# Performance work log

Hardware: AMD Instinct MI355X
Metric: run time of the kernel (lower is better)

The kernel has to match this reference:

```python
import jax, jax.numpy as jnp
import numpy as np

NUM_HEADS = 16
EPS = 1e-5


def _layernorm(x, gamma, beta):
    # LayerNorm over last dim (head_dim), biased variance as in torch
    mu = jnp.mean(x, axis=-1, keepdims=True)
    var = jnp.mean(jnp.square(x - mu), axis=-1, keepdims=True)
    return (x - mu) * jax.lax.rsqrt(var + EPS) * gamma + beta


def setup_inputs() -> dict:
    key = jax.random.key(0)
    ks = jax.random.split(key, 10)
    B, T, C = 16, 2048, 1024
    Bk = 4
    Dh = C // NUM_HEADS
    w = 0.02
    return {
        "q": jax.random.normal(ks[0], (B, T, C), jnp.float32),
        "k": jax.random.normal(ks[1], (Bk, T, C), jnp.float32),
        "v": jax.random.normal(ks[2], (Bk, T, C), jnp.float32),
        "Wq": jax.random.normal(ks[3], (C, C), jnp.float32) * w,
        "Wk": jax.random.normal(ks[4], (C, C), jnp.float32) * w,
        "Wv": jax.random.normal(ks[5], (C, C), jnp.float32) * w,
        "Wo": jax.random.normal(ks[6], (C, C), jnp.float32) * w,
        "bo": jnp.zeros((C,), jnp.float32),
        "gamma": jnp.ones((Dh,), jnp.float32),
        "beta": jnp.zeros((Dh,), jnp.float32),
    }


def reference(q, k, v, Wq, Wk, Wv, Wo, bo, gamma, beta):
    B, N, C = q.shape
    H = NUM_HEADS
    Dh = C // H
    scale = 8.0 / Dh  # use_mup=True

    reps = B // k.shape[0]
    k = jnp.tile(k, (reps, 1, 1))[:, :N]
    v = jnp.tile(v, (reps, 1, 1))[:, :N]

    # torch Linear: x @ W.T  (no qkv bias)
    qp = jnp.einsum("bnc,dc->bnd", q, Wq).reshape(B, N, H, Dh)
    kp = jnp.einsum("bnc,dc->bnd", k, Wk).reshape(B, N, H, Dh)
    vp = jnp.einsum("bnc,dc->bnd", v, Wv).reshape(B, N, H, Dh)

    qp = _layernorm(qp, gamma, beta) * scale
    kp = _layernorm(kp, gamma, beta)

    # Faithful to source: NO head permute before matmul -> per-token (H,H) attention
    attn = jnp.einsum("bnhd,bngd->bnhg", qp, kp)  # [B,N,H,H]
    attn = jax.nn.softmax(attn, axis=-1)
    x = jnp.einsum("bnhg,bngd->bnhd", attn, vp)  # [B,N,H,Dh]
    # torch: transpose(1,2).reshape(B,N,C)
    x = x.transpose(0, 2, 1, 3).reshape(B, N, C)
    return jnp.einsum("bnc,dc->bnd", x, Wo) + bo
```

## Files before the change

kernel.cpp:

```cpp
#include <hip/hip_runtime.h>
#include <stdint.h>

typedef short bf16x8 __attribute__((ext_vector_type(8)));
typedef float f32x4 __attribute__((ext_vector_type(4)));

#define DEVINL static __device__ __forceinline__
#define SB() __builtin_amdgcn_sched_barrier(0)

DEVINL unsigned short f2bf(float f) {
    union { float f; uint32_t u; } v; v.f = f;
    return (unsigned short)((v.u + 0x7FFFu + ((v.u >> 16) & 1u)) >> 16);
}
DEVINL float bf2f(unsigned short b) {
    union { uint32_t u; float f; } v; v.u = ((uint32_t)b) << 16;
    return v.f;
}

DEVINL void load_lds16(const void* g, void* l) {
    __builtin_amdgcn_global_load_lds(
        (const __attribute__((address_space(1))) void*)g,
        (__attribute__((address_space(3))) void*)l, 16, 0, 0);
}

__global__ __launch_bounds__(256) void k_cvtall(
    const float* __restrict__ q, const float* __restrict__ k, const float* __restrict__ v,
    const float* __restrict__ w0, const float* __restrict__ w1,
    const float* __restrict__ w2, const float* __restrict__ w3,
    unsigned short* __restrict__ dq, unsigned short* __restrict__ dk,
    unsigned short* __restrict__ dv,
    unsigned short* __restrict__ dw0, unsigned short* __restrict__ dw1,
    unsigned short* __restrict__ dw2, unsigned short* __restrict__ dw3)
{
    const float* src; unsigned short* dst; int n4, blk, nblk;
    const int b = blockIdx.x;
    if (b < 2048)      { src = q; dst = dq; n4 = 8388608; blk = b;        nblk = 2048; }
    else if (b < 2560) { src = k; dst = dk; n4 = 2097152; blk = b - 2048; nblk = 512; }
    else if (b < 3072) { src = v; dst = dv; n4 = 2097152; blk = b - 2560; nblk = 512; }
    else {
        const int wsel = (b - 3072) >> 6;
        const float* ws_[4] = {w0, w1, w2, w3};
        unsigned short* wd_[4] = {dw0, dw1, dw2, dw3};
        src = ws_[wsel]; dst = wd_[wsel]; n4 = 262144; blk = (b - 3072) & 63; nblk = 64;
    }
    for (int i = blk * 256 + threadIdx.x; i < n4; i += nblk * 256) {
        float4 f = reinterpret_cast<const float4*>(src)[i];
        ushort4 o;
        o.x = f2bf(f.x); o.y = f2bf(f.y); o.z = f2bf(f.z); o.w = f2bf(f.w);
        reinterpret_cast<ushort4*>(dst)[i] = o;
    }
}

#define MFMA_QUAD(mi, nj, av, bv)                                              \
    __builtin_amdgcn_s_setprio(1);                                             \
    _Pragma("unroll")                                                          \
    for (int i = 0; i < 4; ++i)                                                \
        _Pragma("unroll")                                                      \
        for (int j = 0; j < 2; ++j)                                            \
            _Pragma("unroll")                                                  \
            for (int ks = 0; ks < 2; ++ks)                                     \
                acc[(mi) * 4 + i][(nj) * 2 + j] =                              \
                    __builtin_amdgcn_mfma_f32_16x16x32_bf16(                   \
                        av[i][ks], bv[j][ks], acc[(mi)*4+i][(nj)*2+j], 0, 0, 0); \
    __builtin_amdgcn_s_setprio(0);

template<int EPI>
DEVINL void epi_write(f32x4 (&acc)[8][4], void* Cout,
                      const float* bias, const float* gamma, const float* beta,
                      int m0, int n0, int wr, int wc, int lane, int wg)
{
    constexpr int N = 1024;
    const int rr = lane & 15;
    const int rg = lane >> 4;
    if constexpr (EPI == 0) {
        #pragma unroll
        for (int jj = 0; jj < 4; ++jj) {
            const int col = n0 + wc * 64 + jj * 16 + rr;
            const float bv = bias[col];
            #pragma unroll
            for (int i = 0; i < 8; ++i) {
                const int row0 = m0 + wr * 128 + i * 16 + rg * 4;
                #pragma unroll
                for (int r = 0; r < 4; ++r)
                    reinterpret_cast<float*>(Cout)[(size_t)(row0 + r) * N + col] =
                        acc[i][jj][r] + bv;
            }
        }
    } else if constexpr (EPI == 1 || EPI == 3) {
        const float scale = (EPI == 1) ? 0.125f : 1.0f;
        float gm[4], bt[4];
        #pragma unroll
        for (int jj = 0; jj < 4; ++jj) { gm[jj] = gamma[jj * 16 + rr]; bt[jj] = beta[jj * 16 + rr]; }
        #pragma unroll
        for (int i = 0; i < 8; ++i)
            #pragma unroll
            for (int r = 0; r < 4; ++r) {
                float s = 0.f, sq = 0.f;
                #pragma unroll
                for (int jj = 0; jj < 4; ++jj) {
                    const float v = acc[i][jj][r];
                    s += v; sq += v * v;
                }
                s  += __shfl_xor(s, 1);  s  += __shfl_xor(s, 2);
                s  += __shfl_xor(s, 4);  s  += __shfl_xor(s, 8);
                sq += __shfl_xor(sq, 1); sq += __shfl_xor(sq, 2);
                sq += __shfl_xor(sq, 4); sq += __shfl_xor(sq, 8);
                const float mu = s * 0.015625f;
                const float var = sq * 0.015625f - mu * mu;
                const float inv = rsqrtf(var + 1e-5f);
                const int row = m0 + wr * 128 + i * 16 + rg * 4 + r;
                #pragma unroll
                for (int jj = 0; jj < 4; ++jj) {
                    const int col = n0 + wc * 64 + jj * 16 + rr;
                    const float val = ((acc[i][jj][r] - mu) * inv * gm[jj] + bt[jj]) * scale;
                    reinterpret_cast<unsigned short*>(Cout)[(size_t)row * N + col] = f2bf(val);
                }
            }
    } else {
        const int g = (wg & 3) * 4 + wc;
        const int kqv = g >> 3;
        const int ev = g & 7;
        #pragma unroll
        for (int i = 0; i < 8; ++i)
            #pragma unroll
            for (int r = 0; r < 4; ++r) {
                const int t = m0 + wr * 128 + i * 16 + rg * 4 + r;
                #pragma unroll
                for (int jj = 0; jj < 4; ++jj)
                    reinterpret_cast<unsigned short*>(Cout)[
                        (size_t)t * 1024 + jj * 256 + kqv * 128 + rr * 8 + ev] =
                        f2bf(acc[i][jj][r]);
            }
    }
}

#define LOFF(buf, ab, ks, row) (((((buf) * 2 + (ab)) * 2 + (ks)) * 256 + (row)) * 32)

template<int EPI>
DEVINL void gemm256_body(
    const unsigned short* __restrict__ A,
    const unsigned short* __restrict__ B,
    void* __restrict__ Cout,
    const float* __restrict__ bias,
    const float* __restrict__ gamma,
    const float* __restrict__ beta,
    unsigned short* lds, int bid, int nwg, int tid)
{
    constexpr int K = 1024;
    constexpr int NT = 16;

    const int wg  = (bid & 7) * (nwg >> 3) + (bid >> 3);
    const int m0 = (wg >> 2) * 256;
    const int n0 = (wg & 3) * 256;

    const int w = tid >> 6;
    const int lane = tid & 63;
    const int wr = w >> 2;
    const int wc = w & 3;

    const int srow = lane >> 2;
    const int sseg = lane & 3;
    const int sslot = sseg ^ ((srow >> 1) & 3);

    f32x4 acc[8][4] = {};

    auto stage_unit = [&](int buf, int kt, int unit) {
        const int k0 = kt * 64;
        const int ab = unit & 1;
        const int sel = unit >> 1;
        #pragma unroll
        for (int j = 0; j < 2; ++j) {
            const int c  = (w << 1) | j;
            const int ks = c >> 3;
            const int c3 = c & 7;
            const int rg = ab ? (sel * 2 + (c3 & 1) + ((c3 >> 1) << 2))
                              : (sel * 4 + (c3 & 3) + ((c3 >> 2) << 3));
            const int row = rg * 16 + srow;
            const unsigned short* src =
                (ab ? B + (size_t)(n0 + row) * K : A + (size_t)(m0 + row) * K)
                + k0 + ks * 32 + sslot * 8;
            load_lds16(src, lds + LOFF(buf, ab, ks, rg * 16));
        }
    };

    const int rr = lane & 15;
    const int rdslot = ((lane >> 4) ^ ((rr >> 1) & 3)) * 8;

    auto rd_a = [&](bf16x8 (&dst)[4][2], int cur, int mh) {
        #pragma unroll
        for (int i = 0; i < 4; ++i)
            #pragma unroll
            for (int ks = 0; ks < 2; ++ks)
                dst[i][ks] = *reinterpret_cast<const bf16x8*>(
                    lds + LOFF(cur, 0, ks, wr * 128 + mh * 64 + i * 16 + rr) + rdslot);
    };
    auto rd_b = [&](bf16x8 (&dst)[2][2], int cur, int nh) {
        #pragma unroll
        for (int j = 0; j < 2; ++j)
            #pragma unroll
            for (int ks = 0; ks < 2; ++ks)
                dst[j][ks] = *reinterpret_cast<const bf16x8*>(
                    lds + LOFF(cur, 1, ks, wc * 64 + nh * 32 + j * 16 + rr) + rdslot);
    };

    stage_unit(0, 0, 0);
    stage_unit(0, 0, 1);
    stage_unit(0, 0, 3);
    stage_unit(0, 0, 2);
    asm volatile("s_waitcnt vmcnt(4)" ::: "memory");
    __builtin_amdgcn_s_barrier();
    SB();

    bf16x8 a[4][2], b0[2][2], b1[2][2];
    int cur = 0;
    for (int kt = 0; kt < NT - 1; ++kt) {
        const int nxt = cur ^ 1;

        rd_a(a, cur, 0);
        rd_b(b0, cur, 0);
        SB();
        stage_unit(nxt, kt + 1, 0);
        asm volatile("s_waitcnt vmcnt(4)" ::: "memory");
        __builtin_amdgcn_s_barrier();
        SB();
        asm volatile("s_waitcnt lgkmcnt(0)" ::: "memory");
        SB();
        MFMA_QUAD(0, 0, a, b0)

        rd_b(b1, cur, 1);
        SB();
        stage_unit(nxt, kt + 1, 1);
        asm volatile("s_waitcnt vmcnt(4)" ::: "memory");
        __builtin_amdgcn_s_barrier();
        SB();
        asm volatile("s_waitcnt lgkmcnt(0)" ::: "memory");
        SB();
        MFMA_QUAD(0, 1, a, b1)

        rd_a(a, cur, 1);
        SB();
        stage_unit(nxt, kt + 1, 3);
        __builtin_amdgcn_s_barrier();
        SB();
        asm volatile("s_waitcnt lgkmcnt(0)" ::: "memory");
        SB();
        MFMA_QUAD(1, 0, a, b0)

        stage_unit(nxt, kt + 1, 2);
        asm volatile("s_waitcnt vmcnt(4)" ::: "memory");
        __builtin_amdgcn_s_barrier();
        SB();
        MFMA_QUAD(1, 1, a, b1)
        cur = nxt;
    }

    {
        rd_a(a, cur, 0);
        rd_b(b0, cur, 0);
        SB();
        asm volatile("s_waitcnt vmcnt(2)" ::: "memory");
        __builtin_amdgcn_s_barrier();
        SB();
        asm volatile("s_waitcnt lgkmcnt(0)" ::: "memory");
        SB();
        MFMA_QUAD(0, 0, a, b0)

        rd_b(b1, cur, 1);
        SB();
        asm volatile("s_waitcnt vmcnt(0)" ::: "memory");
        __builtin_amdgcn_s_barrier();
        SB();
        asm volatile("s_waitcnt lgkmcnt(0)" ::: "memory");
        SB();
        MFMA_QUAD(0, 1, a, b1)

        rd_a(a, cur, 1);
        SB();
        asm volatile("s_waitcnt lgkmcnt(0)" ::: "memory");
        SB();
        MFMA_QUAD(1, 0, a, b0)
        MFMA_QUAD(1, 1, a, b1)
    }

    epi_write<EPI>(acc, Cout, bias, gamma, beta, m0, n0, wr, wc, lane, wg);
}

#undef MFMA_QUAD

template<int EPI>
__global__ __launch_bounds__(512, 2) void k_gemm256(
    const unsigned short* __restrict__ A,
    const unsigned short* __restrict__ B,
    void* __restrict__ Cout,
    const float* __restrict__ bias,
    const float* __restrict__ gamma,
    const float* __restrict__ beta)
{
    __shared__ __align__(16) unsigned short lds[2 * 2 * 2 * 256 * 32];
    gemm256_body<EPI>(A, B, Cout, bias, gamma, beta, lds, blockIdx.x, gridDim.x, threadIdx.x);
}

__global__ __launch_bounds__(512, 2) void k_gemm256kv(
    const unsigned short* __restrict__ Ak,
    const unsigned short* __restrict__ Bk,
    void* __restrict__ Ck,
    const unsigned short* __restrict__ Av,
    const unsigned short* __restrict__ Bv,
    void* __restrict__ Cv,
    const float* __restrict__ gamma,
    const float* __restrict__ beta)
{
    __shared__ __align__(16) unsigned short lds[2 * 2 * 2 * 256 * 32];
    if (blockIdx.x < 128)
        gemm256_body<3>(Ak, Bk, Ck, nullptr, gamma, beta, lds, blockIdx.x, 128, threadIdx.x);
    else
        gemm256_body<2>(Av, Bv, Cv, nullptr, nullptr, nullptr, lds, blockIdx.x - 128, 128, threadIdx.x);
}

__global__ __launch_bounds__(256) void k_attn2(
    const unsigned short* __restrict__ qln,
    const unsigned short* __restrict__ kln,
    const unsigned short* __restrict__ vperm,
    unsigned short* __restrict__ xout)
{
    __shared__ unsigned short ps[4][256];
    __shared__ unsigned short xs[4][16 * 68];

    const int w = threadIdx.x >> 6;
    const int lane = threadIdx.x & 63;
    const int token = blockIdx.x * 4 + w;
    const int b = token >> 11;
    const int n = token & 2047;
    const int tokk = (b & 3) * 2048 + n;
    const int rr = lane & 15;
    const int kq = lane >> 4;

    const unsigned short* qp = qln + (size_t)token * 1024 + rr * 64 + kq * 8;
    const unsigned short* kp = kln + (size_t)tokk * 1024 + rr * 64 + kq * 8;
    const bf16x8 aq0 = *reinterpret_cast<const bf16x8*>(qp);
    const bf16x8 aq1 = *reinterpret_cast<const bf16x8*>(qp + 32);
    const bf16x8 bk0 = *reinterpret_cast<const bf16x8*>(kp);
    const bf16x8 bk1 = *reinterpret_cast<const bf16x8*>(kp + 32);
    f32x4 s = {};
    s = __builtin_amdgcn_mfma_f32_16x16x32_bf16(aq0, bk0, s, 0, 0, 0);
    s = __builtin_amdgcn_mfma_f32_16x16x32_bf16(aq1, bk1, s, 0, 0, 0);

    #pragma unroll
    for (int r = 0; r < 4; ++r) {
        float m = s[r];
        m = fmaxf(m, __shfl_xor(m, 1));
        m = fmaxf(m, __shfl_xor(m, 2));
        m = fmaxf(m, __shfl_xor(m, 4));
        m = fmaxf(m, __shfl_xor(m, 8));
        const float e = __expf(s[r] - m);
        float t = e;
        t += __shfl_xor(t, 1); t += __shfl_xor(t, 2);
        t += __shfl_xor(t, 4); t += __shfl_xor(t, 8);
        ps[w][(kq * 4 + r) * 16 + rr] = f2bf(e / t);
    }

    bf16x8 ap = {};
    if (kq < 2)
        ap = *reinterpret_cast<const bf16x8*>(&ps[w][rr * 16 + kq * 8]);

    const unsigned short* vp = vperm + (size_t)tokk * 1024;
    #pragma unroll
    for (int dblk = 0; dblk < 4; ++dblk) {
        bf16x8 bv = {};
        if (kq < 2)
            bv = *reinterpret_cast<const bf16x8*>(vp + dblk * 256 + kq * 128 + rr * 8);
        f32x4 z = {};
        const f32x4 x = __builtin_amdgcn_mfma_f32_16x16x32_bf16(ap, bv, z, 0, 0, 0);
        #pragma unroll
        for (int r = 0; r < 4; ++r)
            xs[w][(kq * 4 + r) * 68 + dblk * 16 + rr] = f2bf(x[r]);
    }

    const int h2 = lane >> 2;
    const int sg = lane & 3;
    const uint4 lo = *reinterpret_cast<const uint4*>(&xs[w][h2 * 68 + sg * 16]);
    const uint4 hi = *reinterpret_cast<const uint4*>(&xs[w][h2 * 68 + sg * 16 + 8]);
    unsigned short* dst = xout + (size_t)b * 2048 * 1024 +
                          (size_t)(h2 * 128 + (n >> 4)) * 1024 + (n & 15) * 64 + sg * 16;
    *reinterpret_cast<uint4*>(dst) = lo;
    *reinterpret_cast<uint4*>(dst + 8) = hi;
}

extern "C" void kernel_launch(void* const* d_in, const int* in_sizes, int n_in,
                              void* d_out, int out_size, void* d_ws, size_t ws_size,
                              hipStream_t stream) {
    const float* q     = (const float*)d_in[0];
    const float* k     = (const float*)d_in[1];
    const float* v     = (const float*)d_in[2];
    const float* Wq    = (const float*)d_in[3];
    const float* Wk    = (const float*)d_in[4];
    const float* Wv    = (const float*)d_in[5];
    const float* Wo    = (const float*)d_in[6];
    const float* bo    = (const float*)d_in[7];
    const float* gamma = (const float*)d_in[8];
    const float* beta  = (const float*)d_in[9];
    float* out = (float*)d_out;

    char* ws = (char*)d_ws;
    const size_t MB = 1024 * 1024;
    unsigned short* qb    = (unsigned short*)(ws + 0);
    unsigned short* xsc   = (unsigned short*)(ws + 0);
    unsigned short* qpb   = (unsigned short*)(ws + 64 * MB);
    unsigned short* klnb  = (unsigned short*)(ws + 128 * MB);
    unsigned short* vbb   = (unsigned short*)(ws + 144 * MB);
    unsigned short* vpm   = (unsigned short*)(ws + 160 * MB);
    unsigned short* kbb   = (unsigned short*)(ws + 176 * MB);
    unsigned short* Wkb   = (unsigned short*)(ws + 192 * MB);
    unsigned short* Wvb   = (unsigned short*)(ws + 194 * MB);
    unsigned short* Wqb   = (unsigned short*)(ws + 196 * MB);
    unsigned short* Wob   = (unsigned short*)(ws + 198 * MB);

    k_cvtall<<<3328, 256, 0, stream>>>(q, k, v, Wk, Wv, Wq, Wo,
                                       qb, kbb, vbb, Wkb, Wvb, Wqb, Wob);

    k_gemm256kv<<<256, 512, 0, stream>>>(kbb, Wkb, klnb, vbb, Wvb, vpm, gamma, beta);

    k_gemm256<1><<<512, 512, 0, stream>>>(qb, Wqb, qpb, nullptr, gamma, beta);

    k_attn2<<<8192, 256, 0, stream>>>(qpb, klnb, vpm, xsc);

    k_gemm256<0><<<512, 512, 0, stream>>>(xsc, Wob, out, bo, nullptr, nullptr);
}
```

Measured before the change: 300.1 us.

## Fuse fp32-to-bf16 activation conversion into GEMM A-tile loading

```diff
diff --git a/kernel.cpp b/kernel.cpp
--- a/kernel.cpp
+++ b/kernel.cpp
@@ -11,9 +11,14 @@
     union { float f; uint32_t u; } v; v.f = f;
     return (unsigned short)((v.u + 0x7FFFu + ((v.u >> 16) & 1u)) >> 16);
 }
-DEVINL float bf2f(unsigned short b) {
-    union { uint32_t u; float f; } v; v.u = ((uint32_t)b) << 16;
-    return v.f;
+
+DEVINL bf16x8 cvt8(f32x4 lo, f32x4 hi) {
+    bf16x8 r;
+    r[0] = (short)f2bf(lo[0]); r[1] = (short)f2bf(lo[1]);
+    r[2] = (short)f2bf(lo[2]); r[3] = (short)f2bf(lo[3]);
+    r[4] = (short)f2bf(hi[0]); r[5] = (short)f2bf(hi[1]);
+    r[6] = (short)f2bf(hi[2]); r[7] = (short)f2bf(hi[3]);
+    return r;
 }
 
 DEVINL void load_lds16(const void* g, void* l) {
@@ -22,31 +27,22 @@
         (__attribute__((address_space(3))) void*)l, 16, 0, 0);
 }
 
-__global__ __launch_bounds__(256) void k_cvtall(
-    const float* __restrict__ q, const float* __restrict__ k, const float* __restrict__ v,
-    const float* __restrict__ w0, const float* __restrict__ w1,
-    const float* __restrict__ w2, const float* __restrict__ w3,
-    unsigned short* __restrict__ dq, unsigned short* __restrict__ dk,
-    unsigned short* __restrict__ dv,
-    unsigned short* __restrict__ dw0, unsigned short* __restrict__ dw1,
-    unsigned short* __restrict__ dw2, unsigned short* __restrict__ dw3)
-{
-    const float* src; unsigned short* dst; int n4, blk, nblk;
-    const int b = blockIdx.x;
-    if (b < 2048)      { src = q; dst = dq; n4 = 8388608; blk = b;        nblk = 2048; }
-    else if (b < 2560) { src = k; dst = dk; n4 = 2097152; blk = b - 2048; nblk = 512; }
-    else if (b < 3072) { src = v; dst = dv; n4 = 2097152; blk = b - 2560; nblk = 512; }
-    else {
-        const int wsel = (b - 3072) >> 6;
-        const float* ws_[4] = {w0, w1, w2, w3};
-        unsigned short* wd_[4] = {dw0, dw1, dw2, dw3};
-        src = ws_[wsel]; dst = wd_[wsel]; n4 = 262144; blk = (b - 3072) & 63; nblk = 64;
-    }
-    for (int i = blk * 256 + threadIdx.x; i < n4; i += nblk * 256) {
-        float4 f = reinterpret_cast<const float4*>(src)[i];
-        ushort4 o;
-        o.x = f2bf(f.x); o.y = f2bf(f.y); o.z = f2bf(f.z); o.w = f2bf(f.w);
-        reinterpret_cast<ushort4*>(dst)[i] = o;
+__global__ __launch_bounds__(256) void k_cvtW(
+    const float* __restrict__ s0, const float* __restrict__ s1,
+    const float* __restrict__ s2, const float* __restrict__ s3,
+    unsigned short* __restrict__ d0, unsigned short* __restrict__ d1,
+    unsigned short* __restrict__ d2, unsigned short* __restrict__ d3)
+{
+    const float* srcs[4] = {s0, s1, s2, s3};
+    unsigned short* dsts[4] = {d0, d1, d2, d3};
+    const int wsel = blockIdx.x >> 7;
+    const int blk  = blockIdx.x & 127;
+    const float* src = srcs[wsel];
+    unsigned short* dst = dsts[wsel];
+    for (int i = blk * 256 + threadIdx.x; i < 131072; i += 128 * 256) {
+        const f32x4 f0 = reinterpret_cast<const f32x4*>(src)[2 * i];
+        const f32x4 f1 = reinterpret_cast<const f32x4*>(src)[2 * i + 1];
+        reinterpret_cast<bf16x8*>(dst)[i] = cvt8(f0, f1);
     }
 }
 
@@ -135,9 +131,9 @@
 
 #define LOFF(buf, ab, ks, row) (((((buf) * 2 + (ab)) * 2 + (ks)) * 256 + (row)) * 32)
 
-template<int EPI>
+template<int EPI, int AF32>
 DEVINL void gemm256_body(
-    const unsigned short* __restrict__ A,
+    const void* __restrict__ A,
     const unsigned short* __restrict__ B,
     void* __restrict__ Cout,
     const float* __restrict__ bias,
@@ -161,24 +157,69 @@
     const int sseg = lane & 3;
     const int sslot = sseg ^ ((srow >> 1) & 3);
 
+    const float* Af = (const float*)A;
+    const unsigned short* Ab = (const unsigned short*)A;
+
     f32x4 acc[8][4] = {};
-
-    auto stage_unit = [&](int buf, int kt, int unit) {
+    f32x4 fA[8];
+
+    auto stage_A_gl = [&](int buf, int kt) {
         const int k0 = kt * 64;
-        const int ab = unit & 1;
-        const int sel = unit >> 1;
+        #pragma unroll
+        for (int sel = 0; sel < 2; ++sel)
+            #pragma unroll
+            for (int j = 0; j < 2; ++j) {
+                const int c = (w << 1) | j;
+                const int ks = c >> 3;
+                const int c3 = c & 7;
+                const int rg = sel * 4 + (c3 & 3) + ((c3 >> 2) << 3);
+                const int row = rg * 16 + srow;
+                load_lds16(Ab + (size_t)(m0 + row) * K + k0 + ks * 32 + sslot * 8,
+                           lds + LOFF(buf, 0, ks, rg * 16));
+            }
+    };
+    auto issue_A = [&](int kt) {
+        const int k0 = kt * 64;
+        #pragma unroll
+        for (int sel = 0; sel < 2; ++sel)
+            #pragma unroll
+            for (int j = 0; j < 2; ++j) {
+                const int g = sel * 2 + j;
+                const int c = (w << 1) | j;
+                const int ks = c >> 3;
+                const int c3 = c & 7;
+                const int rg = sel * 4 + (c3 & 3) + ((c3 >> 2) << 3);
+                const int row = rg * 16 + srow;
+                const float* s = Af + (size_t)(m0 + row) * K + k0 + ks * 32 + sslot * 8;
+                fA[2 * g]     = *reinterpret_cast<const f32x4*>(s);
+                fA[2 * g + 1] = *reinterpret_cast<const f32x4*>(s + 4);
+            }
+    };
+    auto write_A = [&](int buf) {
+        #pragma unroll
+        for (int sel = 0; sel < 2; ++sel)
+            #pragma unroll
+            for (int j = 0; j < 2; ++j) {
+                const int g = sel * 2 + j;
+                const int c = (w << 1) | j;
+                const int ks = c >> 3;
+                const int c3 = c & 7;
+                const int rg = sel * 4 + (c3 & 3) + ((c3 >> 2) << 3);
+                *reinterpret_cast<bf16x8*>(lds + LOFF(buf, 0, ks, rg * 16) + lane * 8) =
+                    cvt8(fA[2 * g], fA[2 * g + 1]);
+            }
+    };
+    auto stage_B = [&](int buf, int kt, int sel) {
+        const int k0 = kt * 64;
         #pragma unroll
         for (int j = 0; j < 2; ++j) {
-            const int c  = (w << 1) | j;
+            const int c = (w << 1) | j;
             const int ks = c >> 3;
             const int c3 = c & 7;
-            const int rg = ab ? (sel * 2 + (c3 & 1) + ((c3 >> 1) << 2))
-                              : (sel * 4 + (c3 & 3) + ((c3 >> 2) << 3));
+            const int rg = sel * 2 + (c3 & 1) + ((c3 >> 1) << 2);
             const int row = rg * 16 + srow;
-            const unsigned short* src =
-                (ab ? B + (size_t)(n0 + row) * K : A + (size_t)(m0 + row) * K)
-                + k0 + ks * 32 + sslot * 8;
-            load_lds16(src, lds + LOFF(buf, ab, ks, rg * 16));
+            load_lds16(B + (size_t)(n0 + row) * K + k0 + ks * 32 + sslot * 8,
+                       lds + LOFF(buf, 1, ks, rg * 16));
         }
     };
 
@@ -202,11 +243,14 @@
                     lds + LOFF(cur, 1, ks, wc * 64 + nh * 32 + j * 16 + rr) + rdslot);
     };
 
-    stage_unit(0, 0, 0);
-    stage_unit(0, 0, 1);
-    stage_unit(0, 0, 3);
-    stage_unit(0, 0, 2);
+    if constexpr (AF32) issue_A(0); else stage_A_gl(0, 0);
+    stage_B(0, 0, 0);
+    stage_B(0, 0, 1);
     asm volatile("s_waitcnt vmcnt(4)" ::: "memory");
+    SB();
+    if constexpr (AF32) { write_A(0); SB(); }
+    asm volatile("s_waitcnt lgkmcnt(0)" ::: "memory");
+    SB();
     __builtin_amdgcn_s_barrier();
     SB();
 
@@ -216,59 +260,67 @@
         const int nxt = cur ^ 1;
 
         rd_a(a, cur, 0);
+        SB();
+        if constexpr (AF32) issue_A(kt + 1); else stage_A_gl(nxt, kt + 1);
+        SB();
+        if constexpr (AF32) { asm volatile("s_waitcnt vmcnt(10)" ::: "memory"); }
+        else                { asm volatile("s_waitcnt vmcnt(6)" ::: "memory"); }
+        __builtin_amdgcn_s_barrier();
+        SB();
         rd_b(b0, cur, 0);
         SB();
-        stage_unit(nxt, kt + 1, 0);
+        asm volatile("s_waitcnt lgkmcnt(0)" ::: "memory");
+        SB();
+        MFMA_QUAD(0, 0, a, b0)
+
+        stage_B(nxt, kt + 1, 0);
+        SB();
+        if constexpr (AF32) { asm volatile("s_waitcnt vmcnt(10)" ::: "memory"); }
+        else                { asm volatile("s_waitcnt vmcnt(6)" ::: "memory"); }
+        __builtin_amdgcn_s_barrier();
+        SB();
+        rd_b(b1, cur, 1);
+        SB();
+        asm volatile("s_waitcnt lgkmcnt(0)" ::: "memory");
+        SB();
+        MFMA_QUAD(0, 1, a, b1)
+
+        rd_a(a, cur, 1);
+        SB();
+        stage_B(nxt, kt + 1, 1);
+        SB();
+        asm volatile("s_waitcnt lgkmcnt(0)" ::: "memory");
+        SB();
+        MFMA_QUAD(1, 0, a, b0)
+
         asm volatile("s_waitcnt vmcnt(4)" ::: "memory");
+        SB();
+        if constexpr (AF32) { write_A(nxt); SB(); }
+        MFMA_QUAD(1, 1, a, b1)
+        asm volatile("s_waitcnt lgkmcnt(0)" ::: "memory");
+        SB();
         __builtin_amdgcn_s_barrier();
         SB();
-        asm volatile("s_waitcnt lgkmcnt(0)" ::: "memory");
-        SB();
-        MFMA_QUAD(0, 0, a, b0)
-
-        rd_b(b1, cur, 1);
-        SB();
-        stage_unit(nxt, kt + 1, 1);
-        asm volatile("s_waitcnt vmcnt(4)" ::: "memory");
-        __builtin_amdgcn_s_barrier();
-        SB();
-        asm volatile("s_waitcnt lgkmcnt(0)" ::: "memory");
-        SB();
-        MFMA_QUAD(0, 1, a, b1)
-
-        rd_a(a, cur, 1);
-        SB();
-        stage_unit(nxt, kt + 1, 3);
-        __builtin_amdgcn_s_barrier();
-        SB();
-        asm volatile("s_waitcnt lgkmcnt(0)" ::: "memory");
-        SB();
-        MFMA_QUAD(1, 0, a, b0)
-
-        stage_unit(nxt, kt + 1, 2);
-        asm volatile("s_waitcnt vmcnt(4)" ::: "memory");
-        __builtin_amdgcn_s_barrier();
-        SB();
-        MFMA_QUAD(1, 1, a, b1)
         cur = nxt;
     }
 
     {
         rd_a(a, cur, 0);
-        rd_b(b0, cur, 0);
         SB();
         asm volatile("s_waitcnt vmcnt(2)" ::: "memory");
         __builtin_amdgcn_s_barrier();
         SB();
+        rd_b(b0, cur, 0);
+        SB();
         asm volatile("s_waitcnt lgkmcnt(0)" ::: "memory");
         SB();
         MFMA_QUAD(0, 0, a, b0)
 
-        rd_b(b1, cur, 1);
-        SB();
         asm volatile("s_waitcnt vmcnt(0)" ::: "memory");
         __builtin_amdgcn_s_barrier();
         SB();
+        rd_b(b1, cur, 1);
+        SB();
         asm volatile("s_waitcnt lgkmcnt(0)" ::: "memory");
         SB();
         MFMA_QUAD(0, 1, a, b1)
@@ -286,9 +338,9 @@
 
 #undef MFMA_QUAD
 
-template<int EPI>
+template<int EPI, int AF32>
 __global__ __launch_bounds__(512, 2) void k_gemm256(
-    const unsigned short* __restrict__ A,
+    const void* __restrict__ A,
     const unsigned short* __restrict__ B,
     void* __restrict__ Cout,
     const float* __restrict__ bias,
@@ -296,14 +348,14 @@
     const float* __restrict__ beta)
 {
     __shared__ __align__(16) unsigned short lds[2 * 2 * 2 * 256 * 32];
-    gemm256_body<EPI>(A, B, Cout, bias, gamma, beta, lds, blockIdx.x, gridDim.x, threadIdx.x);
+    gemm256_body<EPI, AF32>(A, B, Cout, bias, gamma, beta, lds, blockIdx.x, gridDim.x, threadIdx.x);
 }
 
 __global__ __launch_bounds__(512, 2) void k_gemm256kv(
-    const unsigned short* __restrict__ Ak,
+    const float* __restrict__ Ak,
     const unsigned short* __restrict__ Bk,
     void* __restrict__ Ck,
-    const unsigned short* __restrict__ Av,
+    const float* __restrict__ Av,
     const unsigned short* __restrict__ Bv,
     void* __restrict__ Cv,
     const float* __restrict__ gamma,
@@ -311,9 +363,9 @@
 {
     __shared__ __align__(16) unsigned short lds[2 * 2 * 2 * 256 * 32];
     if (blockIdx.x < 128)
-        gemm256_body<3>(Ak, Bk, Ck, nullptr, gamma, beta, lds, blockIdx.x, 128, threadIdx.x);
+        gemm256_body<3, 1>(Ak, Bk, Ck, nullptr, gamma, beta, lds, blockIdx.x, 128, threadIdx.x);
     else
-        gemm256_body<2>(Av, Bv, Cv, nullptr, nullptr, nullptr, lds, blockIdx.x - 128, 128, threadIdx.x);
+        gemm256_body<2, 1>(Av, Bv, Cv, nullptr, nullptr, nullptr, lds, blockIdx.x - 128, 128, threadIdx.x);
 }
 
 __global__ __launch_bounds__(256) void k_attn2(
@@ -402,26 +454,22 @@
 
     char* ws = (char*)d_ws;
     const size_t MB = 1024 * 1024;
-    unsigned short* qb    = (unsigned short*)(ws + 0);
     unsigned short* xsc   = (unsigned short*)(ws + 0);
     unsigned short* qpb   = (unsigned short*)(ws + 64 * MB);
     unsigned short* klnb  = (unsigned short*)(ws + 128 * MB);
-    unsigned short* vbb   = (unsigned short*)(ws + 144 * MB);
-    unsigned short* vpm   = (unsigned short*)(ws + 160 * MB);
-    unsigned short* kbb   = (unsigned short*)(ws + 176 * MB);
-    unsigned short* Wkb   = (unsigned short*)(ws + 192 * MB);
-    unsigned short* Wvb   = (unsigned short*)(ws + 194 * MB);
-    unsigned short* Wqb   = (unsigned short*)(ws + 196 * MB);
-    unsigned short* Wob   = (unsigned short*)(ws + 198 * MB);
-
-    k_cvtall<<<3328, 256, 0, stream>>>(q, k, v, Wk, Wv, Wq, Wo,
-                                       qb, kbb, vbb, Wkb, Wvb, Wqb, Wob);
-
-    k_gemm256kv<<<256, 512, 0, stream>>>(kbb, Wkb, klnb, vbb, Wvb, vpm, gamma, beta);
-
-    k_gemm256<1><<<512, 512, 0, stream>>>(qb, Wqb, qpb, nullptr, gamma, beta);
+    unsigned short* vpm   = (unsigned short*)(ws + 144 * MB);
+    unsigned short* Wkb   = (unsigned short*)(ws + 160 * MB);
+    unsigned short* Wvb   = (unsigned short*)(ws + 162 * MB);
+    unsigned short* Wqb   = (unsigned short*)(ws + 164 * MB);
+    unsigned short* Wob   = (unsigned short*)(ws + 166 * MB);
+
+    k_cvtW<<<512, 256, 0, stream>>>(Wk, Wv, Wq, Wo, Wkb, Wvb, Wqb, Wob);
+
+    k_gemm256kv<<<256, 512, 0, stream>>>(k, Wkb, klnb, v, Wvb, vpm, gamma, beta);
+
+    k_gemm256<1, 1><<<512, 512, 0, stream>>>(q, Wqb, qpb, nullptr, gamma, beta);
 
     k_attn2<<<8192, 256, 0, stream>>>(qpb, klnb, vpm, xsc);
 
-    k_gemm256<0><<<512, 512, 0, stream>>>(xsc, Wob, out, bo, nullptr, nullptr);
-}
+    k_gemm256<0, 0><<<512, 512, 0, stream>>>(xsc, Wob, out, bo, nullptr, nullptr);
+}
```

Result: slower. 351.2 us (+17.0%).
